# Kernel optimization log

Measured on AMD Instinct MI355X. Metric: run time of the kernel, lower is better.

Reference implementation:

```python
import jax, jax.numpy as jnp
import numpy as np

B, T, D, H, L = 2, 1000, 768, 12, 2
DK = D // H
MLP_HID = D * 1  # mlp_ratio = 1
WIDTHS = [7, 15, 31, 63, 127, 255, 7, 15, 31, 63, 127, 255]


def _band_mask():
    # diagonal_mask(seq_len, mask_width): True = blocked (outside the diagonal band)
    i = np.arange(T)[:, None]
    j = np.arange(T)[None, :]
    m = np.stack([np.abs(i - j) > (w // 2) for w in WIDTHS], 0)  # (H, T, T)
    return jnp.asarray(m)


def _rel_pos_emb():
    # espnet-style RelPositionalEncoding: rel positions T-1 .. -(T-1), shape (2T-1, D)
    pos = jnp.arange(T - 1, -T, -1, dtype=jnp.float32)
    div = jnp.exp(jnp.arange(0, D, 2, dtype=jnp.float32) * (-np.log(10000.0) / D))
    ang = pos[:, None] * div[None, :]
    return jnp.stack([jnp.sin(ang), jnp.cos(ang)], -1).reshape(2 * T - 1, D)


def setup_inputs() -> dict:
    key = jax.random.key(0)
    ks = iter(jax.random.split(key, 32))
    rn = lambda sh, s=0.02: jax.random.normal(next(ks), sh, jnp.float32) * s
    return {
        "x": jax.random.normal(next(ks), (B, T, D), jnp.float32),
        "mask": _band_mask(),
        "ln1_g": jnp.ones((L, D)), "ln1_b": jnp.zeros((L, D)),
        "wq": rn((L, D, D)), "bq": jnp.zeros((L, D)),
        "wk": rn((L, D, D)), "bk": jnp.zeros((L, D)),
        "wv": rn((L, D, D)), "bv": jnp.zeros((L, D)),
        "wo": rn((L, D, D)), "bo": jnp.zeros((L, D)),
        "wpos": rn((L, D, D)),
        "pbu": rn((L, H, DK)), "pbv": rn((L, H, DK)),
        "ln2_g": jnp.ones((L, D)), "ln2_b": jnp.zeros((L, D)),
        "w1": rn((L, D, MLP_HID)), "b1": jnp.zeros((L, MLP_HID)),
        "w2": rn((L, MLP_HID, D)), "b2": jnp.zeros((L, D)),
    }


def _ln(x, g, b):
    m = jnp.mean(x, -1, keepdims=True)
    v = jnp.var(x, -1, keepdims=True)
    return (x - m) * jax.lax.rsqrt(v + 1e-5) * g + b


def _rel_shift(x):
    # x: (b, h, t, 2t-1) -> shifted so column s corresponds to rel pos (t-1 - s + row offset)
    b, h, t, n = x.shape
    x = jnp.pad(x, ((0, 0), (0, 0), (0, 0), (1, 0)))        # (b,h,t,2t)
    x = x.reshape(b, h, n + 1, t)[:, :, 1:, :].reshape(b, h, t, n)
    return x[..., :t]


def _forward(x, mask, p):
    (ln1_g, ln1_b, wq, bq, wk, bk, wv, bv, wo, bo,
     wpos, pbu, pbv, ln2_g, ln2_b, w1, b1, w2, b2) = p
    pe = _rel_pos_emb()                                      # (2T-1, D)
    x = x * jnp.asarray(np.sqrt(D), x.dtype)                 # xscale in RelPositionalEncoding
    neg = jnp.asarray(-1e30, x.dtype)
    inv_sqrt_dk = 1.0 / np.sqrt(DK)
    for l in range(L):
        h = _ln(x, ln1_g[l], ln1_b[l])
        q = (h @ wq[l] + bq[l]).reshape(B, T, H, DK)
        k = (h @ wk[l] + bk[l]).reshape(B, T, H, DK)
        v = (h @ wv[l] + bv[l]).reshape(B, T, H, DK)
        pp = (pe @ wpos[l]).reshape(2 * T - 1, H, DK)        # pos projection (no bias)
        ac = jnp.einsum('bthd,bshd->bhts', q + pbu[l], k)    # content term
        bd = _rel_shift(jnp.einsum('bthd,nhd->bhtn', q + pbv[l], pp))  # position term
        s = (ac + bd) * inv_sqrt_dk
        s = jnp.where(mask[None], neg, s)                    # per-head diagonal band mask
        a = jax.nn.softmax(s, axis=-1)
        o = jnp.einsum('bhts,bshd->bthd', a, v).reshape(B, T, D) @ wo[l] + bo[l]
        x = x + o
        h2 = _ln(x, ln2_g[l], ln2_b[l])
        x = x + (jax.nn.gelu(h2 @ w1[l] + b1[l], approximate=False) @ w2[l] + b2[l])
    return x


def reference(x, mask, ln1_g, ln1_b, wq, bq, wk, bk, wv, bv, wo, bo, wpos, pbu, pbv, ln2_g, ln2_b, w1, b1, w2, b2):
    return _forward(x, mask, (ln1_g, ln1_b, wq, bq, wk, bk, wv, bv, wo, bo,
                              wpos, pbu, pbv, ln2_g, ln2_b, w1, b1, w2, b2))
```

## Files before the change

### kernel.cpp

```cpp
#include <hip/hip_runtime.h>

#define TT 1000
#define BB 2
#define DD 768
#define HH 12
#define DK 64
#define LL 2
#define WELEM 589824
#define PEROWS 255
#define VTP 1312
#define PPL 195840

typedef __bf16 bf16x8 __attribute__((ext_vector_type(8)));
typedef float floatx4 __attribute__((ext_vector_type(4)));

__device__ __constant__ int HALFW[12] = {3,7,15,31,63,127,3,7,15,31,63,127};
__device__ __constant__ int HORD[12]  = {5,11,4,10,3,9,2,8,1,7,0,6};

__device__ __forceinline__ float b2f(unsigned short u){
    union { unsigned int i; float f; } x; x.i = ((unsigned int)u) << 16; return x.f;
}
__device__ __forceinline__ unsigned short f2b(float f){
    union { float f; unsigned int i; } x; x.f = f;
    unsigned int i = x.i;
    i += 0x7fffu + ((i >> 16) & 1u);
    return (unsigned short)(i >> 16);
}
__device__ __forceinline__ void gload16(const void* g, void* l){
    __builtin_amdgcn_global_load_lds(
        (const __attribute__((address_space(1))) void*)g,
        (__attribute__((address_space(3))) void*)l, 16, 0, 0);
}

__global__ __launch_bounds__(256)
void prep_kernel(const float* s0, const float* s1, const float* s2, const float* s3,
                 const float* s4, const float* s5, const float* s6,
                 unsigned short* __restrict__ dst,
                 const float* __restrict__ x, float* __restrict__ xc,
                 unsigned short* __restrict__ pe){
    int z = blockIdx.z;
    int tid = threadIdx.x;
    if (z < 14){
        const float* srcs[7] = {s0,s1,s2,s3,s4,s5,s6};
        const float* src = srcs[z % 7] + (size_t)(z / 7)*WELEM;
        unsigned short* d = dst + (size_t)z*WELEM;
        int k0 = blockIdx.x*64, n0 = blockIdx.y*64;
        __shared__ __align__(16) unsigned short tile[64][72];
        int r = tid >> 2, c = tid & 3;
        const float4* sp = (const float4*)(src + (size_t)(k0+r)*DD + n0 + c*16);
        float4 f0 = sp[0], f1 = sp[1], f2 = sp[2], f3 = sp[3];
        unsigned short u[16];
        u[0]=f2b(f0.x); u[1]=f2b(f0.y); u[2]=f2b(f0.z); u[3]=f2b(f0.w);
        u[4]=f2b(f1.x); u[5]=f2b(f1.y); u[6]=f2b(f1.z); u[7]=f2b(f1.w);
        u[8]=f2b(f2.x); u[9]=f2b(f2.y); u[10]=f2b(f2.z); u[11]=f2b(f2.w);
        u[12]=f2b(f3.x); u[13]=f2b(f3.y); u[14]=f2b(f3.z); u[15]=f2b(f3.w);
        *(int4*)&tile[r][c*16]   = *(int4*)&u[0];
        *(int4*)&tile[r][c*16+8] = *(int4*)&u[8];
        __syncthreads();
        unsigned short tmp[16];
        #pragma unroll
        for (int i=0;i<16;++i) tmp[i] = tile[c*16+i][r];
        int4* dp = (int4*)(d + (size_t)(n0+r)*DD + k0 + c*16);
        dp[0] = *(int4*)&tmp[0];
        dp[1] = *(int4*)&tmp[8];
    } else if (z == 14){
        int id = blockIdx.y*12 + blockIdx.x;
        for (int i = id*256 + tid; i < 384000; i += 36864){
            float4 v = ((const float4*)x)[i];
            v.x *= 27.712812921102035f; v.y *= 27.712812921102035f;
            v.z *= 27.712812921102035f; v.w *= 27.712812921102035f;
            ((float4*)xc)[i] = v;
        }
    } else {
        int bid = blockIdx.y*12 + blockIdx.x;
        #pragma unroll
        for (int rr = 0; rr < 2; ++rr){
            int row = bid*2 + rr;
            if (row < PEROWS){
                float pos = (float)(127 - row);
                int i = tid;
                float dv = expf((float)(2*i) * (-9.210340371976184f / 768.0f));
                float ang = pos * dv;
                pe[(size_t)row*DD + 2*i]   = f2b(sinf(ang));
                pe[(size_t)row*DD + 2*i+1] = f2b(cosf(ang));
                if (tid < 128){
                    int j = 256 + tid;
                    float dv2 = expf((float)(2*j) * (-9.210340371976184f / 768.0f));
                    float an2 = pos * dv2;
                    pe[(size_t)row*DD + 2*j]   = f2b(sinf(an2));
                    pe[(size_t)row*DD + 2*j+1] = f2b(cosf(an2));
                }
            }
        }
    }
}

__global__ __launch_bounds__(256)
void ln_kernel(const float* __restrict__ x, const float* __restrict__ g,
               const float* __restrict__ bb, unsigned short* __restrict__ out){
    int row = blockIdx.x;
    const float* xr = x + (size_t)row*DD;
    int tid = threadIdx.x;
    float v0 = xr[tid], v1 = xr[tid+256], v2 = xr[tid+512];
    float s = v0+v1+v2, ss = v0*v0+v1*v1+v2*v2;
    #pragma unroll
    for (int o=1;o<64;o<<=1){ s += __shfl_xor(s,o); ss += __shfl_xor(ss,o); }
    __shared__ float rs[4], rss[4];
    int wv = tid>>6, lane = tid&63;
    if (lane==0){ rs[wv]=s; rss[wv]=ss; }
    __syncthreads();
    s  = rs[0]+rs[1]+rs[2]+rs[3];
    ss = rss[0]+rss[1]+rss[2]+rss[3];
    float mean = s * (1.0f/768.0f);
    float var  = ss * (1.0f/768.0f) - mean*mean;
    float inv  = 1.0f / sqrtf(var + 1e-5f);
    unsigned short* orow = out + (size_t)row*DD;
    #pragma unroll
    for (int kk=0;kk<3;++kk){
        int i = tid + 256*kk;
        float v = (kk==0?v0:(kk==1?v1:v2));
        orow[i] = f2b((v - mean)*inv*g[i] + bb[i]);
    }
}

#define GEMM_GL64(A_, Bt_, n0_, M_)                                             \
    int tid = threadIdx.x;                                                      \
    int m0 = blockIdx.x*64;                                                     \
    int wv = tid>>6, lane = tid&63;                                             \
    int quad = lane>>4, l16 = lane&15;                                          \
    floatx4 acc[4];                                                             \
    _Pragma("unroll")                                                           \
    for (int ni=0;ni<4;++ni) acc[ni] = (floatx4){0.f,0.f,0.f,0.f};              \
    {                                                                           \
      int rl0 = wv*16 + (lane>>3);                                              \
      int rl1 = rl0 + 8;                                                        \
      int gc  = (lane&7) ^ (lane>>3);                                           \
      int ra0 = m0 + rl0; if (ra0 > (M_)-1) ra0 = (M_)-1;                       \
      int ra1 = m0 + rl1; if (ra1 > (M_)-1) ra1 = (M_)-1;                       \
      const char* gA0 = (const char*)(A_)  + (size_t)ra0*1536 + gc*16;          \
      const char* gA1 = (const char*)(A_)  + (size_t)ra1*1536 + gc*16;          \
      const char* gB0 = (const char*)(Bt_) + (size_t)((n0_)+rl0)*1536 + gc*16;  \
      const char* gB1 = (const char*)(Bt_) + (size_t)((n0_)+rl1)*1536 + gc*16;  \
      char* shB = (char*)sh;                                                    \
      int ld0 = (2*wv)*1024, ld1 = (2*wv+1)*1024;                               \
      int arow = (16*wv + l16)*64;                                              \
      int sw8  = l16 & 7;                                                       \
      int cq0 = (quad ^ sw8)*8;                                                 \
      int cq1 = ((4|quad) ^ sw8)*8;                                             \
      gload16(gA0, shB + ld0);                                                  \
      gload16(gA1, shB + ld1);                                                  \
      gload16(gB0, shB + 8192 + ld0);                                           \
      gload16(gB1, shB + 8192 + ld1);                                           \
      for (int s=0; s<12; ++s){                                                 \
        if (s < 11){                                                            \
          char* nb = shB + ((s+1)&1)*16384;                                     \
          int off = (s+1)*128;                                                  \
          gload16(gA0 + off, nb + ld0);                                         \
          gload16(gA1 + off, nb + ld1);                                         \
          gload16(gB0 + off, nb + 8192 + ld0);                                  \
          gload16(gB1 + off, nb + 8192 + ld1);                                  \
          asm volatile("s_waitcnt vmcnt(4)" ::: "memory");                      \
        } else {                                                                \
          asm volatile("s_waitcnt vmcnt(0)" ::: "memory");                      \
        }                                                                       \
        __builtin_amdgcn_s_barrier();                                           \
        __builtin_amdgcn_sched_barrier(0);                                      \
        const unsigned short* cA = sh + (s&1)*8192;                             \
        const unsigned short* cB = cA + 4096;                                   \
        _Pragma("unroll")                                                       \
        for (int kh=0; kh<2; ++kh){                                             \
          int cq = kh ? cq1 : cq0;                                              \
          bf16x8 af = *(const bf16x8*)&cA[arow + cq];                           \
          _Pragma("unroll")                                                     \
          for (int ni=0; ni<4; ++ni){                                           \
            bf16x8 bfv = *(const bf16x8*)&cB[ni*1024 + l16*64 + cq];            \
            acc[ni] = __builtin_amdgcn_mfma_f32_16x16x32_bf16(af, bfv, acc[ni], 0,0,0); \
          }                                                                     \
        }                                                                       \
        __builtin_amdgcn_sched_barrier(0);                                      \
        __builtin_amdgcn_s_barrier();                                           \
      }                                                                         \
    }

#define GEMM_GL64_3B(A_, Bt_, n0_, M_)                                          \
    int tid = threadIdx.x;                                                      \
    int m0 = blockIdx.x*64;                                                     \
    int wv = tid>>6, lane = tid&63;                                             \
    int quad = lane>>4, l16 = lane&15;                                          \
    floatx4 acc[4];                                                             \
    _Pragma("unroll")                                                           \
    for (int ni=0;ni<4;++ni) acc[ni] = (floatx4){0.f,0.f,0.f,0.f};              \
    {                                                                           \
      int rl0 = wv*16 + (lane>>3);                                              \
      int rl1 = rl0 + 8;                                                        \
      int gc  = (lane&7) ^ (lane>>3);                                           \
      int ra0 = m0 + rl0; if (ra0 > (M_)-1) ra0 = (M_)-1;                       \
      int ra1 = m0 + rl1; if (ra1 > (M_)-1) ra1 = (M_)-1;                       \
      const char* gA0 = (const char*)(A_)  + (size_t)ra0*1536 + gc*16;          \
      const char* gA1 = (const char*)(A_)  + (size_t)ra1*1536 + gc*16;          \
      const char* gB0 = (const char*)(Bt_) + (size_t)((n0_)+rl0)*1536 + gc*16;  \
      const char* gB1 = (const char*)(Bt_) + (size_t)((n0_)+rl1)*1536 + gc*16;  \
      char* shB = (char*)sh;                                                    \
      int ld0 = (2*wv)*1024, ld1 = (2*wv+1)*1024;                               \
      int arow = (16*wv + l16)*64;                                              \
      int sw8  = l16 & 7;                                                       \
      int cq0 = (quad ^ sw8)*8;                                                 \
      int cq1 = ((4|quad) ^ sw8)*8;                                             \
      gload16(gA0, shB + ld0);                                                  \
      gload16(gA1, shB + ld1);                                                  \
      gload16(gB0, shB + 8192 + ld0);                                           \
      gload16(gB1, shB + 8192 + ld1);                                           \
      gload16(gA0 + 128, shB + 16384 + ld0);                                    \
      gload16(gA1 + 128, shB + 16384 + ld1);                                    \
      gload16(gB0 + 128, shB + 16384 + 8192 + ld0);                             \
      gload16(gB1 + 128, shB + 16384 + 8192 + ld1);                             \
      for (int s=0; s<12; ++s){                                                 \
        if (s < 11) asm volatile("s_waitcnt vmcnt(4)" ::: "memory");            \
        else        asm volatile("s_waitcnt vmcnt(0)" ::: "memory");            \
        __builtin_amdgcn_s_barrier();                                           \
        __builtin_amdgcn_sched_barrier(0);                                      \
        if (s < 10){                                                            \
          char* nb = shB + ((s+2)%3)*16384;                                     \
          int off = (s+2)*128;                                                  \
          gload16(gA0 + off, nb + ld0);                                         \
          gload16(gA1 + off, nb + ld1);                                         \
          gload16(gB0 + off, nb + 8192 + ld0);                                  \
          gload16(gB1 + off, nb + 8192 + ld1);                                  \
        }                                                                       \
        __builtin_amdgcn_sched_barrier(0);                                      \
        const unsigned short* cA = sh + (s%3)*8192;                             \
        const unsigned short* cB = cA + 4096;                                   \
        _Pragma("unroll")                                                       \
        for (int kh=0; kh<2; ++kh){                                             \
          int cq = kh ? cq1 : cq0;                                              \
          bf16x8 af = *(const bf16x8*)&cA[arow + cq];                           \
          _Pragma("unroll")                                                     \
          for (int ni=0; ni<4; ++ni){                                           \
            bf16x8 bfv = *(const bf16x8*)&cB[ni*1024 + l16*64 + cq];            \
            acc[ni] = __builtin_amdgcn_mfma_f32_16x16x32_bf16(af, bfv, acc[ni], 0,0,0); \
          }                                                                     \
        }                                                                       \
        __builtin_amdgcn_sched_barrier(0);                                      \
      }                                                                         \
    }

template<int MODE>
__global__ __launch_bounds__(256)
void gemm_kernel(const unsigned short* __restrict__ A, const unsigned short* __restrict__ Bt,
                 const float* __restrict__ bias, unsigned short* __restrict__ outb,
                 float* __restrict__ resid, int M){
    __shared__ __align__(16) unsigned short sh[24576];
    int n0 = blockIdx.y*64;
    GEMM_GL64_3B(A, Bt, n0, M)
    float bfv_[4];
    #pragma unroll
    for (int ni=0;ni<4;++ni) bfv_[ni] = bias ? bias[n0 + 16*ni + l16] : 0.0f;
    #pragma unroll
    for (int rr=0;rr<4;++rr){
        int row = m0 + 16*wv + 4*quad + rr;
        if (row >= M) continue;
        #pragma unroll
        for (int ni=0;ni<4;++ni){
            int col = n0 + 16*ni + l16;
            float v = acc[ni][rr] + bfv_[ni];
            if (MODE == 1)      outb[(size_t)row*768 + col] = f2b(0.5f*v*(1.0f + erff(v*0.70710678118654752f)));
            else                resid[(size_t)row*768 + col] += v;
        }
    }
}

__global__ __launch_bounds__(256)
void gemm_pos_kernel(const unsigned short* __restrict__ A, const unsigned short* __restrict__ Bt,
                     unsigned short* __restrict__ outb){
    __shared__ __align__(16) unsigned short sh[24576];
    int n0 = blockIdx.y*64;
    int zz = blockIdx.z;
    const unsigned short* Bt_ = Bt + (size_t)zz*7*WELEM;
    unsigned short* outb_ = outb + (size_t)zz*PPL;
    GEMM_GL64_3B(A, Bt_, n0, PEROWS)
    #pragma unroll
    for (int rr=0;rr<4;++rr){
        int row = m0 + 16*wv + 4*quad + rr;
        if (row >= PEROWS) continue;
        #pragma unroll
        for (int ni=0;ni<4;++ni){
            int col = n0 + 16*ni + l16;
            int h = col >> 6, d = col & 63;
            outb_[((size_t)h*PEROWS + row)*DK + d] = f2b(acc[ni][rr]);
        }
    }
}

__global__ __launch_bounds__(256)
void gemm_qkv_kernel(const unsigned short* __restrict__ A, const unsigned short* __restrict__ Bt,
                     const float* __restrict__ bq, const float* __restrict__ bk, const float* __restrict__ bv,
                     unsigned short* __restrict__ qout, unsigned short* __restrict__ kout,
                     unsigned short* __restrict__ vout){
    __shared__ __align__(16) unsigned short sh[16384];
    int n0 = blockIdx.y*64;
    GEMM_GL64(A, Bt, n0, 2000)
    int sec = blockIdx.y / 12;
    int col0 = n0 - sec*768;
    int h = col0 >> 6;
    const float* bias = (sec==0) ? bq : (sec==1) ? bk : bv;
    float bfv_[4];
    #pragma unroll
    for (int ni=0;ni<4;++ni) bfv_[ni] = bias[col0 + 16*ni + l16];
    if (sec != 2){
        unsigned short* outp = (sec==0) ? qout : kout;
        #pragma unroll
        for (int rr=0;rr<4;++rr){
            int row = m0 + 16*wv + 4*quad + rr;
            if (row >= 2000) continue;
            int b = row / TT, tl = row - b*TT;
            #pragma unroll
            for (int ni=0;ni<4;++ni){
                int d = 16*ni + l16;
                outp[(((size_t)(b*HH + h))*TT + tl)*DK + d] = f2b(acc[ni][rr] + bfv_[ni]);
            }
        }
    } else {
        #pragma unroll
        for (int rr=0;rr<4;++rr){
            int rt = 16*wv + 4*quad + rr;
            #pragma unroll
            for (int ni=0;ni<4;++ni)
                sh[rt*66 + 16*ni + l16] = f2b(acc[ni][rr] + bfv_[ni]);
        }
        __syncthreads();
        #pragma unroll
        for (int it=0; it<16; ++it){
            int idx = it*256 + tid;
            int d = idx >> 6, rt = idx & 63;
            int row = m0 + rt;
            if (row < 2000){
                int b = row / TT, tl = row - b*TT;
                vout[(((size_t)(b*HH + h))*DK + d)*VTP + tl + 128] = sh[rt*66 + d];
            }
        }
    }
}

__global__ __launch_bounds__(256)
void attn_kernel(const unsigned short* __restrict__ q, const unsigned short* __restrict__ k,
                 const unsigned short* __restrict__ vT, const unsigned short* __restrict__ pp,
                 const float* __restrict__ pbu, const float* __restrict__ pbv,
                 unsigned short* __restrict__ out){
    int b = blockIdx.y, h = HORD[blockIdx.z];
    int t0 = blockIdx.x * 16;
    int w2 = HALFW[h];
    int tid = threadIdx.x;
    int wv = tid >> 6, lane = tid & 63;
    int l16 = lane & 15, quad = lane >> 4;

    const unsigned short* qB = q  + ((size_t)(b*HH + h))*TT*DK;
    const unsigned short* kB = k  + ((size_t)(b*HH + h))*TT*DK;
    const unsigned short* vB = vT + ((size_t)(b*HH + h))*DK*VTP;
    const unsigned short* pB = pp + (size_t)h*PEROWS*DK;

    __shared__ __align__(16) float bd[16*260];
    __shared__ __align__(16) unsigned short pl[16*328];
    __shared__ float sms[4][16];

    int tq = t0 + l16; if (tq > TT-1) tq = TT-1;
    union { int4 i; unsigned short u[8]; } r0, r1;
    r0.i = *(const int4*)(qB + (size_t)tq*DK + quad*8);
    r1.i = *(const int4*)(qB + (size_t)tq*DK + 32 + quad*8);
    const float* pu = pbu + h*DK + quad*8;
    const float* pv = pbv + h*DK + quad*8;
    union { unsigned short u[8]; bf16x8 v; } qu0, qu1, qv0, qv1;
    #pragma unroll
    for (int i=0;i<8;++i){
        float a0 = b2f(r0.u[i]), a1 = b2f(r1.u[i]);
        qu0.u[i] = f2b(a0 + pu[i]);
        qu1.u[i] = f2b(a1 + pu[32+i]);
        qv0.u[i] = f2b(a0 + pv[i]);
        qv1.u[i] = f2b(a1 + pv[32+i]);
    }

    int Nn = 2*w2 + 1;
    int ntiles = (Nn + 15) >> 4;
    for (int ti = wv; ti < ntiles; ti += 4){
        int n = 127 - w2 + ti*16 + l16; if (n > PEROWS-1) n = PEROWS-1;
        const unsigned short* pr = pB + (size_t)n*DK + quad*8;
        bf16x8 pb0 = *(const bf16x8*)pr;
        bf16x8 pb1 = *(const bf16x8*)(pr + 32);
        floatx4 a = {0.f,0.f,0.f,0.f};
        a = __builtin_amdgcn_mfma_f32_16x16x32_bf16(qv0.v, pb0, a, 0,0,0);
        a = __builtin_amdgcn_mfma_f32_16x16x32_bf16(qv1.v, pb1, a, 0,0,0);
        #pragma unroll
        for (int r=0;r<4;++r) bd[(quad*4+r)*260 + ti*16 + l16] = a[r];
    }
    for (int i = tid; i < 16*328/4; i += 256)
        ((unsigned long long*)pl)[i] = 0ULL;
    __syncthreads();

    int Ns = 2*w2 + 16;
    int stiles = (Ns + 15) >> 4;
    int s_lo = t0 - w2;
    float scv[5][4];
    #pragma unroll
    for (int ii = 0; ii < 5; ++ii){
        int ti = wv + ii*4;
        if (ti < stiles){
            int s = s_lo + ti*16 + l16;
            int sc = s < 0 ? 0 : (s > TT-1 ? TT-1 : s);
            const unsigned short* kr = kB + (size_t)sc*DK + quad*8;
            bf16x8 kb0 = *(const bf16x8*)kr;
            bf16x8 kb1 = *(const bf16x8*)(kr + 32);
            floatx4 a = {0.f,0.f,0.f,0.f};
            a = __builtin_amdgcn_mfma_f32_16x16x32_bf16(qu0.v, kb0, a, 0,0,0);
            a = __builtin_amdgcn_mfma_f32_16x16x32_bf16(qu1.v, kb1, a, 0,0,0);
            #pragma unroll
            for (int r=0;r<4;++r){
                int row = quad*4 + r;
                int nrel = ti*16 + l16 - row;
                bool ok = (nrel >= 0) && (nrel <= 2*w2) && (s >= 0) && (s <= TT-1);
                int idx = row*260 + nrel;
                idx = idx < 0 ? 0 : (idx > 16*260-1 ? 16*260-1 : idx);
                float bdv = bd[idx];
                scv[ii][r] = ok ? (a[r] + bdv) * 0.125f : -1e30f;
            }
        } else {
            #pragma unroll
            for (int r=0;r<4;++r) scv[ii][r] = -1e30f;
        }
    }

    float sm[4] = {0.f,0.f,0.f,0.f};
    #pragma unroll
    for (int ii = 0; ii < 5; ++ii){
        int ti = wv + ii*4;
        if (ti < stiles){
            int pad_base = (t0 - w2) - ((t0 - w2) & ~31);
            #pragma unroll
            for (int r=0;r<4;++r){
                float e = __expf(scv[ii][r]);
                sm[r] += e;
                pl[(quad*4+r)*328 + pad_base + ti*16 + l16] = f2b(e);
            }
        }
    }
    #pragma unroll
    for (int off=1; off<16; off<<=1){
        #pragma unroll
        for (int r=0;r<4;++r) sm[r] += __shfl_xor(sm[r], off);
    }
    if (l16 == 0){
        #pragma unroll
        for (int r=0;r<4;++r) sms[wv][quad*4+r] = sm[r];
    }
    __syncthreads();

    int s_lo2 = t0 - w2;
    int s0a = s_lo2 & ~31;
    int pad_lo = s_lo2 - s0a;
    int ktiles = (pad_lo + Ns + 31) >> 5;

    floatx4 oacc = {0.f,0.f,0.f,0.f};
    for (int kt = 0; kt < ktiles; ++kt){
        bf16x8 pa = *(const bf16x8*)&pl[l16*328 + kt*32 + quad*8];
        int sidx = s0a + kt*32 + quad*8 + 128;
        bf16x8 vb = *(const bf16x8*)(vB + (size_t)(wv*16 + l16)*VTP + sidx);
        oacc = __builtin_amdgcn_mfma_f32_16x16x32_bf16(pa, vb, oacc, 0,0,0);
    }
    #pragma unroll
    for (int r=0;r<4;++r){
        int row = quad*4 + r;
        float sum = sms[0][row] + sms[1][row] + sms[2][row] + sms[3][row];
        float rinv = sum > 0.f ? 1.0f/sum : 0.0f;
        int t = t0 + row;
        if (t <= TT-1)
            out[(((size_t)(b*TT + t))*HH + h)*DK + wv*16 + l16] = f2b(oacc[r] * rinv);
    }
}

extern "C" void kernel_launch(void* const* d_in, const int* in_sizes, int n_in,
                              void* d_out, int out_size, void* d_ws, size_t ws_size,
                              hipStream_t stream){
    const float* x    = (const float*)d_in[0];
    const float* ln1g = (const float*)d_in[2];
    const float* ln1b = (const float*)d_in[3];
    const float* wq   = (const float*)d_in[4];
    const float* bq   = (const float*)d_in[5];
    const float* wk   = (const float*)d_in[6];
    const float* bk   = (const float*)d_in[7];
    const float* wvv  = (const float*)d_in[8];
    const float* bv   = (const float*)d_in[9];
    const float* wo   = (const float*)d_in[10];
    const float* bo   = (const float*)d_in[11];
    const float* wpos = (const float*)d_in[12];
    const float* pbu  = (const float*)d_in[13];
    const float* pbv  = (const float*)d_in[14];
    const float* ln2g = (const float*)d_in[15];
    const float* ln2b = (const float*)d_in[16];
    const float* w1   = (const float*)d_in[17];
    const float* b1   = (const float*)d_in[18];
    const float* w2   = (const float*)d_in[19];
    const float* b2   = (const float*)d_in[20];

    const int NTOK = BB*TT;

    float* x_cur = (float*)d_out;

    char* ws = (char*)d_ws;
    unsigned short* qbuf  = (unsigned short*)(ws);
    unsigned short* kbuf  = (unsigned short*)(ws + 3072000);
    unsigned short* vTbuf = (unsigned short*)(ws + 6144000);
    unsigned short* hbuf  = (unsigned short*)(ws + 10174464);
    unsigned short* ppbuf = (unsigned short*)(ws + 13246464);
    unsigned short* pebuf = (unsigned short*)(ws + 14029824);
    unsigned short* wtbuf = (unsigned short*)(ws + 14421504);
    #define WT(t_,l_) (wtbuf + (size_t)((l_)*7 + (t_))*WELEM)

    dim3 blk(256);
    prep_kernel<<<dim3(12,12,16), blk, 0, stream>>>(wq, wk, wvv, wo, wpos, w1, w2,
                                                    wtbuf, x, x_cur, pebuf);
    gemm_pos_kernel<<<dim3(4,12,2), blk, 0, stream>>>(pebuf, WT(4,0), ppbuf);

    dim3 gBig(32, 12);
    dim3 gQKV(32, 36);
    dim3 gAttn(63, BB, HH);

    for (int l = 0; l < LL; ++l){
        long dl = (long)l*DD;
        long pl_ = (long)l*HH*DK;

        ln_kernel<<<NTOK, blk, 0, stream>>>(x_cur, ln1g + dl, ln1b + dl, hbuf);
        gemm_qkv_kernel<<<gQKV, blk, 0, stream>>>(hbuf, WT(0,l), bq + dl, bk + dl, bv + dl,
                                                  qbuf, kbuf, vTbuf);

        attn_kernel<<<gAttn, blk, 0, stream>>>(qbuf, kbuf, vTbuf, ppbuf + (size_t)l*PPL,
                                               pbu + pl_, pbv + pl_, hbuf);

        gemm_kernel<2><<<gBig, blk, 0, stream>>>(hbuf, WT(3,l), bo + dl, nullptr, x_cur, NTOK);

        ln_kernel<<<NTOK, blk, 0, stream>>>(x_cur, ln2g + dl, ln2b + dl, hbuf);
        gemm_kernel<1><<<gBig, blk, 0, stream>>>(hbuf, WT(5,l), b1 + dl, qbuf, nullptr, NTOK);
        gemm_kernel<2><<<gBig, blk, 0, stream>>>(qbuf, WT(6,l), b2 + dl, nullptr, x_cur, NTOK);
    }
}
```

Before: 282.6 us.

## Fuse LayerNorms into GEMM epilogues and prep, merge pos GEMM into QKV

Removes the standalone LayerNorm launches. The first LN is computed inside the prep kernel's input-scaling path. Later LNs run in the residual GEMM epilogue: the last block to finish a row tile, found through an atomic counter, normalises the updated residual rows. The positional-projection GEMM is also folded into the layer-0 QKV launch as extra blocks, so the forward pass needs fewer kernel launches and fewer separate activation passes. In exchange it adds threadfence/atomic serialization and a tail where one block per row tile does the LN work. It also reuses the PE buffer as counter storage, which attn_kernel resets.

```diff
diff --git a/kernel.cpp b/kernel.cpp
--- a/kernel.cpp
+++ b/kernel.cpp
@@ -37,7 +37,9 @@
                  const float* s4, const float* s5, const float* s6,
                  unsigned short* __restrict__ dst,
                  const float* __restrict__ x, float* __restrict__ xc,
-                 unsigned short* __restrict__ pe){
+                 unsigned short* __restrict__ pe,
+                 const float* __restrict__ lg0, const float* __restrict__ lb0,
+                 unsigned short* __restrict__ ln0out){
     int z = blockIdx.z;
     int tid = threadIdx.x;
     if (z < 14){
@@ -64,12 +66,46 @@
         dp[0] = *(int4*)&tmp[0];
         dp[1] = *(int4*)&tmp[8];
     } else if (z == 14){
-        int id = blockIdx.y*12 + blockIdx.x;
-        for (int i = id*256 + tid; i < 384000; i += 36864){
-            float4 v = ((const float4*)x)[i];
-            v.x *= 27.712812921102035f; v.y *= 27.712812921102035f;
-            v.z *= 27.712812921102035f; v.w *= 27.712812921102035f;
-            ((float4*)xc)[i] = v;
+        int bid = blockIdx.y*12 + blockIdx.x;
+        int wv = tid>>6, lane = tid&63;
+        const float SCL = 27.712812921102035f;
+        #pragma unroll
+        for (int it = 0; it < 4; ++it){
+            int rr = it*4 + wv;
+            if (rr < 14){
+                int row = bid*14 + rr;
+                if (row < 2000){
+                    const float4* xr = (const float4*)x + (size_t)row*192;
+                    float4* xcr = (float4*)xc + (size_t)row*192;
+                    float4 vv[3];
+                    float s = 0.f, ss = 0.f;
+                    #pragma unroll
+                    for (int j=0;j<3;++j){
+                        float4 vq = xr[lane + 64*j];
+                        vq.x *= SCL; vq.y *= SCL; vq.z *= SCL; vq.w *= SCL;
+                        vv[j] = vq;
+                        s  += vq.x+vq.y+vq.z+vq.w;
+                        ss += vq.x*vq.x+vq.y*vq.y+vq.z*vq.z+vq.w*vq.w;
+                        xcr[lane + 64*j] = vq;
+                    }
+                    #pragma unroll
+                    for (int o=1;o<64;o<<=1){ s += __shfl_xor(s,o); ss += __shfl_xor(ss,o); }
+                    float mean = s*(1.0f/768.0f);
+                    float var  = ss*(1.0f/768.0f) - mean*mean;
+                    float inv  = 1.0f/sqrtf(var + 1e-5f);
+                    unsigned short* orow = ln0out + (size_t)row*768;
+                    #pragma unroll
+                    for (int j=0;j<3;++j){
+                        int i0 = (lane + 64*j)*4;
+                        unsigned short o4[4];
+                        o4[0] = f2b((vv[j].x-mean)*inv*lg0[i0]   + lb0[i0]);
+                        o4[1] = f2b((vv[j].y-mean)*inv*lg0[i0+1] + lb0[i0+1]);
+                        o4[2] = f2b((vv[j].z-mean)*inv*lg0[i0+2] + lb0[i0+2]);
+                        o4[3] = f2b((vv[j].w-mean)*inv*lg0[i0+3] + lb0[i0+3]);
+                        *(unsigned long long*)&orow[i0] = *(unsigned long long*)o4;
+                    }
+                }
+            }
         }
     } else {
         int bid = blockIdx.y*12 + blockIdx.x;
@@ -95,37 +131,9 @@
     }
 }
 
-__global__ __launch_bounds__(256)
-void ln_kernel(const float* __restrict__ x, const float* __restrict__ g,
-               const float* __restrict__ bb, unsigned short* __restrict__ out){
-    int row = blockIdx.x;
-    const float* xr = x + (size_t)row*DD;
-    int tid = threadIdx.x;
-    float v0 = xr[tid], v1 = xr[tid+256], v2 = xr[tid+512];
-    float s = v0+v1+v2, ss = v0*v0+v1*v1+v2*v2;
-    #pragma unroll
-    for (int o=1;o<64;o<<=1){ s += __shfl_xor(s,o); ss += __shfl_xor(ss,o); }
-    __shared__ float rs[4], rss[4];
-    int wv = tid>>6, lane = tid&63;
-    if (lane==0){ rs[wv]=s; rss[wv]=ss; }
-    __syncthreads();
-    s  = rs[0]+rs[1]+rs[2]+rs[3];
-    ss = rss[0]+rss[1]+rss[2]+rss[3];
-    float mean = s * (1.0f/768.0f);
-    float var  = ss * (1.0f/768.0f) - mean*mean;
-    float inv  = 1.0f / sqrtf(var + 1e-5f);
-    unsigned short* orow = out + (size_t)row*DD;
-    #pragma unroll
-    for (int kk=0;kk<3;++kk){
-        int i = tid + 256*kk;
-        float v = (kk==0?v0:(kk==1?v1:v2));
-        orow[i] = f2b((v - mean)*inv*g[i] + bb[i]);
-    }
-}
-
-#define GEMM_GL64(A_, Bt_, n0_, M_)                                             \
+#define GEMM_GL64(A_, Bt_, M0_, n0_, M_)                                        \
     int tid = threadIdx.x;                                                      \
-    int m0 = blockIdx.x*64;                                                     \
+    int m0 = (M0_);                                                             \
     int wv = tid>>6, lane = tid&63;                                             \
     int quad = lane>>4, l16 = lane&15;                                          \
     floatx4 acc[4];                                                             \
@@ -182,9 +190,9 @@
       }                                                                         \
     }
 
-#define GEMM_GL64_3B(A_, Bt_, n0_, M_)                                          \
+#define GEMM_GL64_3B(A_, Bt_, M0_, n0_, M_)                                     \
     int tid = threadIdx.x;                                                      \
-    int m0 = blockIdx.x*64;                                                     \
+    int m0 = (M0_);                                                             \
     int wv = tid>>6, lane = tid&63;                                             \
     int quad = lane>>4, l16 = lane&15;                                          \
     floatx4 acc[4];                                                             \
@@ -248,10 +256,12 @@
 __global__ __launch_bounds__(256)
 void gemm_kernel(const unsigned short* __restrict__ A, const unsigned short* __restrict__ Bt,
                  const float* __restrict__ bias, unsigned short* __restrict__ outb,
-                 float* __restrict__ resid, int M){
+                 float* __restrict__ resid, int M,
+                 const float* __restrict__ lng, const float* __restrict__ lnb,
+                 unsigned short* __restrict__ lnout, int* __restrict__ cnt){
     __shared__ __align__(16) unsigned short sh[24576];
     int n0 = blockIdx.y*64;
-    GEMM_GL64_3B(A, Bt, n0, M)
+    GEMM_GL64_3B(A, Bt, blockIdx.x*64, n0, M)
     float bfv_[4];
     #pragma unroll
     for (int ni=0;ni<4;++ni) bfv_[ni] = bias ? bias[n0 + 16*ni + l16] : 0.0f;
@@ -267,26 +277,38 @@
             else                resid[(size_t)row*768 + col] += v;
         }
     }
-}
-
-__global__ __launch_bounds__(256)
-void gemm_pos_kernel(const unsigned short* __restrict__ A, const unsigned short* __restrict__ Bt,
-                     unsigned short* __restrict__ outb){
-    __shared__ __align__(16) unsigned short sh[24576];
-    int n0 = blockIdx.y*64;
-    int zz = blockIdx.z;
-    const unsigned short* Bt_ = Bt + (size_t)zz*7*WELEM;
-    unsigned short* outb_ = outb + (size_t)zz*PPL;
-    GEMM_GL64_3B(A, Bt_, n0, PEROWS)
-    #pragma unroll
-    for (int rr=0;rr<4;++rr){
-        int row = m0 + 16*wv + 4*quad + rr;
-        if (row >= PEROWS) continue;
-        #pragma unroll
-        for (int ni=0;ni<4;++ni){
-            int col = n0 + 16*ni + l16;
-            int h = col >> 6, d = col & 63;
-            outb_[((size_t)h*PEROWS + row)*DK + d] = f2b(acc[ni][rr]);
+    if (MODE == 2 && lnout){
+        __threadfence();
+        __syncthreads();
+        __shared__ int oldc;
+        if (tid == 0) oldc = atomicAdd(cnt + blockIdx.x, 1);
+        __syncthreads();
+        if (oldc == (int)gridDim.y - 1){
+            __threadfence();
+            for (int it = 0; it < 16; ++it){
+                int row = m0 + it*4 + wv;
+                if (row < M){
+                    const float* xr = resid + (size_t)row*768;
+                    float v[12]; float s = 0.f, ss = 0.f;
+                    #pragma unroll
+                    for (int j=0;j<12;++j){
+                        float t = xr[lane + 64*j];
+                        v[j] = t; s += t; ss += t*t;
+                    }
+                    #pragma unroll
+                    for (int o=1;o<64;o<<=1){ s += __shfl_xor(s,o); ss += __shfl_xor(ss,o); }
+                    float mean = s*(1.0f/768.0f);
+                    float var  = ss*(1.0f/768.0f) - mean*mean;
+                    float inv  = 1.0f/sqrtf(var + 1e-5f);
+                    unsigned short* orow = lnout + (size_t)row*768;
+                    #pragma unroll
+                    for (int j=0;j<12;++j){
+                        int i = lane + 64*j;
+                        orow[i] = f2b((v[j]-mean)*inv*lng[i] + lnb[i]);
+                    }
+                }
+            }
+            if (tid == 0) atomicExch(cnt + blockIdx.x, 0);
         }
     }
 }
@@ -295,47 +317,71 @@
 void gemm_qkv_kernel(const unsigned short* __restrict__ A, const unsigned short* __restrict__ Bt,
                      const float* __restrict__ bq, const float* __restrict__ bk, const float* __restrict__ bv,
                      unsigned short* __restrict__ qout, unsigned short* __restrict__ kout,
-                     unsigned short* __restrict__ vout){
+                     unsigned short* __restrict__ vout,
+                     const unsigned short* __restrict__ peA, const unsigned short* __restrict__ posBt,
+                     unsigned short* __restrict__ ppout){
     __shared__ __align__(16) unsigned short sh[16384];
-    int n0 = blockIdx.y*64;
-    GEMM_GL64(A, Bt, n0, 2000)
-    int sec = blockIdx.y / 12;
-    int col0 = n0 - sec*768;
-    int h = col0 >> 6;
-    const float* bias = (sec==0) ? bq : (sec==1) ? bk : bv;
-    float bfv_[4];
-    #pragma unroll
-    for (int ni=0;ni<4;++ni) bfv_[ni] = bias[col0 + 16*ni + l16];
-    if (sec != 2){
-        unsigned short* outp = (sec==0) ? qout : kout;
+    int bid = blockIdx.x;
+    if (bid < 1152){
+        int ny = bid >> 5;
+        int n0 = ny * 64;
+        GEMM_GL64(A, Bt, (bid & 31)*64, n0, 2000)
+        int sec = ny / 12;
+        int col0 = n0 - sec*768;
+        int h = col0 >> 6;
+        const float* bias = (sec==0) ? bq : (sec==1) ? bk : bv;
+        float bfv_[4];
+        #pragma unroll
+        for (int ni=0;ni<4;++ni) bfv_[ni] = bias[col0 + 16*ni + l16];
+        if (sec != 2){
+            unsigned short* outp = (sec==0) ? qout : kout;
+            #pragma unroll
+            for (int rr=0;rr<4;++rr){
+                int row = m0 + 16*wv + 4*quad + rr;
+                if (row >= 2000) continue;
+                int b = row / TT, tl = row - b*TT;
+                #pragma unroll
+                for (int ni=0;ni<4;++ni){
+                    int d = 16*ni + l16;
+                    outp[(((size_t)(b*HH + h))*TT + tl)*DK + d] = f2b(acc[ni][rr] + bfv_[ni]);
+                }
+            }
+        } else {
+            #pragma unroll
+            for (int rr=0;rr<4;++rr){
+                int rt = 16*wv + 4*quad + rr;
+                #pragma unroll
+                for (int ni=0;ni<4;++ni)
+                    sh[rt*66 + 16*ni + l16] = f2b(acc[ni][rr] + bfv_[ni]);
+            }
+            __syncthreads();
+            #pragma unroll
+            for (int it=0; it<16; ++it){
+                int idx = it*256 + tid;
+                int d = idx >> 6, rt = idx & 63;
+                int row = m0 + rt;
+                if (row < 2000){
+                    int b = row / TT, tl = row - b*TT;
+                    vout[(((size_t)(b*HH + h))*DK + d)*VTP + tl + 128] = sh[rt*66 + d];
+                }
+            }
+        }
+    } else {
+        int pid = bid - 1152;
+        int pz = pid / 48, rem = pid % 48;
+        int pn0 = (rem >> 2) * 64;
+        const unsigned short* Bt_ = posBt + (size_t)pz*7*WELEM;
+        unsigned short* outb_ = ppout + (size_t)pz*PPL;
+        GEMM_GL64(peA, Bt_, (rem & 3)*64, pn0, PEROWS)
         #pragma unroll
         for (int rr=0;rr<4;++rr){
             int row = m0 + 16*wv + 4*quad + rr;
-            if (row >= 2000) continue;
-            int b = row / TT, tl = row - b*TT;
+            if (row >= PEROWS) continue;
             #pragma unroll
             for (int ni=0;ni<4;++ni){
-                int d = 16*ni + l16;
-                outp[(((size_t)(b*HH + h))*TT + tl)*DK + d] = f2b(acc[ni][rr] + bfv_[ni]);
-            }
-        }
-    } else {
-        #pragma unroll
-        for (int rr=0;rr<4;++rr){
-            int rt = 16*wv + 4*quad + rr;
-            #pragma unroll
-            for (int ni=0;ni<4;++ni)
-                sh[rt*66 + 16*ni + l16] = f2b(acc[ni][rr] + bfv_[ni]);
-        }
-        __syncthreads();
-        #pragma unroll
-        for (int it=0; it<16; ++it){
-            int idx = it*256 + tid;
-            int d = idx >> 6, rt = idx & 63;
-            int row = m0 + rt;
-            if (row < 2000){
-                int b = row / TT, tl = row - b*TT;
-                vout[(((size_t)(b*HH + h))*DK + d)*VTP + tl + 128] = sh[rt*66 + d];
+                int col = pn0 + 16*ni + l16;
+                int h = col >> 6, d = col & 63;
+                outb_[((size_t)h*PEROWS + row)*DK + d] = f2b(acc[ni][rr]);
             }
         }
     }
@@ -345,13 +391,16 @@
 void attn_kernel(const unsigned short* __restrict__ q, const unsigned short* __restrict__ k,
                  const unsigned short* __restrict__ vT, const unsigned short* __restrict__ pp,
                  const float* __restrict__ pbu, const float* __restrict__ pbv,
-                 unsigned short* __restrict__ out){
+                 unsigned short* __restrict__ out, int* __restrict__ cnt){
     int b = blockIdx.y, h = HORD[blockIdx.z];
     int t0 = blockIdx.x * 16;
     int w2 = HALFW[h];
     int tid = threadIdx.x;
     int wv = tid >> 6, lane = tid & 63;
     int l16 = lane & 15, quad = lane >> 4;
+
+    if (blockIdx.x == 0 && blockIdx.y == 0 && blockIdx.z == 0 && tid < 32)
+        atomicExch(cnt + tid, 0);
 
     const unsigned short* qB = q  + ((size_t)(b*HH + h))*TT*DK;
     const unsigned short* kB = k  + ((size_t)(b*HH + h))*TT*DK;
@@ -511,32 +560,40 @@
     unsigned short* ppbuf = (unsigned short*)(ws + 13246464);
     unsigned short* pebuf = (unsigned short*)(ws + 14029824);
     unsigned short* wtbuf = (unsigned short*)(ws + 14421504);
+    int* cnt = (int*)pebuf;
     #define WT(t_,l_) (wtbuf + (size_t)((l_)*7 + (t_))*WELEM)
 
     dim3 blk(256);
     prep_kernel<<<dim3(12,12,16), blk, 0, stream>>>(wq, wk, wvv, wo, wpos, w1, w2,
-                                                    wtbuf, x, x_cur, pebuf);
-    gemm_pos_kernel<<<dim3(4,12,2), blk, 0, stream>>>(pebuf, WT(4,0), ppbuf);
+                                                    wtbuf, x, x_cur, pebuf,
+                                                    ln1g, ln1b, hbuf);
 
     dim3 gBig(32, 12);
-    dim3 gQKV(32, 36);
     dim3 gAttn(63, BB, HH);
 
     for (int l = 0; l < LL; ++l){
         long dl = (long)l*DD;
         long pl_ = (long)l*HH*DK;
 
-        ln_kernel<<<NTOK, blk, 0, stream>>>(x_cur, ln1g + dl, ln1b + dl, hbuf);
-        gemm_qkv_kernel<<<gQKV, blk, 0, stream>>>(hbuf, WT(0,l), bq + dl, bk + dl, bv + dl,
-                                                  qbuf, kbuf, vTbuf);
+        int nqkv = (l == 0) ? 1248 : 1152;
+        gemm_qkv_kernel<<<dim3(nqkv), blk, 0, stream>>>(hbuf, WT(0,l), bq + dl, bk + dl, bv + dl,
+                                                        qbuf, kbuf, vTbuf,
+                                                        pebuf, WT(4,0), ppbuf);
 
         attn_kernel<<<gAttn, blk, 0, stream>>>(qbuf, kbuf, vTbuf, ppbuf + (size_t)l*PPL,
-                                               pbu + pl_, pbv + pl_, hbuf);
-
-        gemm_kernel<2><<<gBig, blk, 0, stream>>>(hbuf, WT(3,l), bo + dl, nullptr, x_cur, NTOK);
-
-        ln_kernel<<<NTOK, blk, 0, stream>>>(x_cur, ln2g + dl, ln2b + dl, hbuf);
-        gemm_kernel<1><<<gBig, blk, 0, stream>>>(hbuf, WT(5,l), b1 + dl, qbuf, nullptr, NTOK);
-        gemm_kernel<2><<<gBig, blk, 0, stream>>>(qbuf, WT(6,l), b2 + dl, nullptr, x_cur, NTOK);
-    }
-}
+                                               pbu + pl_, pbv + pl_, hbuf, cnt);
+
+        gemm_kernel<2><<<gBig, blk, 0, stream>>>(hbuf, WT(3,l), bo + dl, nullptr, x_cur, NTOK,
+                                                 ln2g + dl, ln2b + dl, hbuf, cnt);
+
+        gemm_kernel<1><<<gBig, blk, 0, stream>>>(hbuf, WT(5,l), b1 + dl, qbuf, nullptr, NTOK,
+                                                 nullptr, nullptr, nullptr, nullptr);
+
+        if (l == 0)
+            gemm_kernel<2><<<gBig, blk, 0, stream>>>(qbuf, WT(6,l), b2 + dl, nullptr, x_cur, NTOK,
+                                                     ln1g + DD, ln1b + DD, hbuf, cnt);
+        else
+            gemm_kernel<2><<<gBig, blk, 0, stream>>>(qbuf, WT(6,l), b2 + dl, nullptr, x_cur, NTOK,
+                                                     nullptr, nullptr, nullptr, nullptr);
+    }
+}
```

Result: slower. 420.5 us (+48.8%).
